# Performance work log

Hardware: AMD Instinct MI355X
Metric: run time of the kernel (lower is better)

## Reference

```python
import jax, jax.numpy as jnp
import numpy as np

EPS = 1e-16  # PyG softmax eps
NEG_SLOPE = 0.2


def _gat_conv(x, W, att_src, att_dst, bias, src, dst, num_nodes, heads, ch, concat):
    # add self loops (PyG default add_self_loops=True)
    loop = jnp.arange(num_nodes, dtype=src.dtype)
    src = jnp.concatenate([src, loop])
    dst = jnp.concatenate([dst, loop])

    h = (x @ W).reshape(num_nodes, heads, ch)          # [N,H,C]
    a_src = jnp.sum(h * att_src, axis=-1)              # [N,H]
    a_dst = jnp.sum(h * att_dst, axis=-1)              # [N,H]

    e = a_src[src] + a_dst[dst]                        # [E,H]
    e = jnp.where(e > 0, e, NEG_SLOPE * e)             # leaky_relu

    # segment softmax over edges grouped by destination node
    m = jax.ops.segment_max(e, dst, num_segments=num_nodes)
    e = jnp.exp(e - m[dst])
    s = jax.ops.segment_sum(e, dst, num_segments=num_nodes)
    alpha = e / (s[dst] + EPS)                          # [E,H]

    msg = h[src] * alpha[:, :, None]                    # [E,H,C]
    out = jax.ops.segment_sum(msg, dst, num_segments=num_nodes)  # [N,H,C]

    if concat:
        out = out.reshape(num_nodes, heads * ch)
    else:
        out = out.mean(axis=1)
    return out + bias


def setup_inputs() -> dict:
    key = jax.random.key(0)
    ks = jax.random.split(key, 12)
    N, E = 50000, 800000
    C_in, C_hid, C_out, H = 128, 32, 64, 8

    x = jax.random.normal(ks[0], (N, C_in), dtype=jnp.float32)
    edge_index = jax.random.randint(ks[1], (2, E), 0, N, dtype=jnp.int64)
    edge_weight = jax.random.uniform(ks[2], (E,), dtype=jnp.float32)

    g = lambda k, shape, fan: jax.random.normal(k, shape, dtype=jnp.float32) * (1.0 / np.sqrt(fan))
    W1 = g(ks[3], (C_in, H * C_hid), C_in)
    att_src1 = g(ks[4], (H, C_hid), C_hid)
    att_dst1 = g(ks[5], (H, C_hid), C_hid)
    bias1 = jnp.zeros((H * C_hid,), dtype=jnp.float32)
    W2 = g(ks[6], (H * C_hid, C_out), H * C_hid)
    att_src2 = g(ks[7], (1, C_out), C_out)
    att_dst2 = g(ks[8], (1, C_out), C_out)
    bias2 = jnp.zeros((C_out,), dtype=jnp.float32)

    return {"x": x, "edge_index": edge_index, "edge_weight": edge_weight,
            "W1": W1, "att_src1": att_src1, "att_dst1": att_dst1, "bias1": bias1,
            "W2": W2, "att_src2": att_src2, "att_dst2": att_dst2, "bias2": bias2}


def reference(x, edge_index, edge_weight, W1, att_src1, att_dst1, bias1,
              W2, att_src2, att_dst2, bias2):
    N = x.shape[0]
    src, dst = edge_index[0], edge_index[1]
    # edge_weight is ignored: GATConv has edge_dim=None, so edge_attr contributes nothing
    h = _gat_conv(x, W1, att_src1, att_dst1, bias1, src, dst, N, 8, 32, concat=True)
    h = jax.nn.elu(h)
    out = _gat_conv(h, W2, att_src2, att_dst2, bias2, src, dst, N, 1, 64, concat=False)
    return out
```

## Files before the change

kernel.cpp:

```cpp
#include <hip/hip_runtime.h>
#include <hip/hip_fp16.h>
#include <math.h>


#define LEAKY(e) ((e) > 0.f ? (e) : 0.2f * (e))
#define CAP 64
#define NPART 2
#define NPB 25000
#define NPW 12500
#define CS 16384

struct __align__(8) H4 { __half2 a, b; };

typedef _Float16 half8 __attribute__((ext_vector_type(8)));
typedef float f32x4 __attribute__((ext_vector_type(4)));

__global__ __launch_bounds__(256) void k1_kernel(
    const int* __restrict__ ei, unsigned* __restrict__ Hg,
    const float* __restrict__ x,
    const float* __restrict__ W1, _Float16* __restrict__ h1h,
    const float* __restrict__ att_src1, const float* __restrict__ att_dst1,
    float* __restrict__ a_src1, float* __restrict__ a_dst1, int N, int E,
    int B, int hblocks) {
  __shared__ __align__(16) unsigned sraw[NPW];
  int t = threadIdx.x, b = blockIdx.x;
  if (b < hblocks) {
    int chunk = b >> 1, p = b & 1;
    for (int i = t; i < NPW; i += 256) sraw[i] = 0u;
    __syncthreads();
    int base = chunk * CS;
    int pbase = p * NPB;
    for (int j = 0; j < CS; j += 256) {
      int idx = base + j + t;
      if (idx < E) {
        int d = ei[E + idx];
        unsigned dl = (unsigned)(d - pbase);
        if (dl < NPB) atomicAdd(&sraw[dl >> 1], 1u << ((dl & 1) * 16));
      }
    }
    __syncthreads();
    unsigned* Hs = Hg + (size_t)(p * B + chunk) * NPW;
    for (int i = t; i < NPW; i += 256) Hs[i] = sraw[i];
    return;
  }
  _Float16* Bs = (_Float16*)sraw;
  int bx = b - hblocks;
  int cb = bx & 3;
  int c0 = cb * 64;
  int w = t >> 6, l = t & 63;
  int lm = l & 15, lq = l >> 4;
  {
    int n = t & 63;
    int kw = t >> 6;
#pragma unroll 8
    for (int i = 0; i < 32; i++) {
      int k = i * 4 + kw;
      Bs[n * 136 + k] = (_Float16)W1[k * 256 + c0 + n];
    }
  }
  __syncthreads();
  int m0 = (bx >> 2) * 128 + w * 32;
  int ra = m0 + lm;      if (ra > N - 1) ra = N - 1;
  int rb = m0 + 16 + lm; if (rb > N - 1) rb = N - 1;
  f32x4 acc[2][4];
#pragma unroll
  for (int mt = 0; mt < 2; mt++)
#pragma unroll
    for (int nt = 0; nt < 4; nt++) acc[mt][nt] = (f32x4){0.f, 0.f, 0.f, 0.f};
  for (int k0 = 0; k0 < 128; k0 += 32) {
    const float* pa = x + (size_t)ra * 128 + k0 + lq * 8;
    const float* pb = x + (size_t)rb * 128 + k0 + lq * 8;
    float4 u0 = *(const float4*)pa, u1 = *(const float4*)(pa + 4);
    float4 w0 = *(const float4*)pb, w1 = *(const float4*)(pb + 4);
    half8 a0, a1;
    a0[0] = (_Float16)u0.x; a0[1] = (_Float16)u0.y;
    a0[2] = (_Float16)u0.z; a0[3] = (_Float16)u0.w;
    a0[4] = (_Float16)u1.x; a0[5] = (_Float16)u1.y;
    a0[6] = (_Float16)u1.z; a0[7] = (_Float16)u1.w;
    a1[0] = (_Float16)w0.x; a1[1] = (_Float16)w0.y;
    a1[2] = (_Float16)w0.z; a1[3] = (_Float16)w0.w;
    a1[4] = (_Float16)w1.x; a1[5] = (_Float16)w1.y;
    a1[6] = (_Float16)w1.z; a1[7] = (_Float16)w1.w;
    half8 b0 = *(const half8*)(Bs + (0 + lm) * 136 + k0 + lq * 8);
    half8 b1 = *(const half8*)(Bs + (16 + lm) * 136 + k0 + lq * 8);
    half8 b2 = *(const half8*)(Bs + (32 + lm) * 136 + k0 + lq * 8);
    half8 b3 = *(const half8*)(Bs + (48 + lm) * 136 + k0 + lq * 8);
    acc[0][0] = __builtin_amdgcn_mfma_f32_16x16x32_f16(a0, b0, acc[0][0], 0, 0, 0);
    acc[0][1] = __builtin_amdgcn_mfma_f32_16x16x32_f16(a0, b1, acc[0][1], 0, 0, 0);
    acc[0][2] = __builtin_amdgcn_mfma_f32_16x16x32_f16(a0, b2, acc[0][2], 0, 0, 0);
    acc[0][3] = __builtin_amdgcn_mfma_f32_16x16x32_f16(a0, b3, acc[0][3], 0, 0, 0);
    acc[1][0] = __builtin_amdgcn_mfma_f32_16x16x32_f16(a1, b0, acc[1][0], 0, 0, 0);
    acc[1][1] = __builtin_amdgcn_mfma_f32_16x16x32_f16(a1, b1, acc[1][1], 0, 0, 0);
    acc[1][2] = __builtin_amdgcn_mfma_f32_16x16x32_f16(a1, b2, acc[1][2], 0, 0, 0);
    acc[1][3] = __builtin_amdgcn_mfma_f32_16x16x32_f16(a1, b3, acc[1][3], 0, 0, 0);
  }
  float as_[4], ad_[4];
#pragma unroll
  for (int nt = 0; nt < 4; nt++) {
    as_[nt] = att_src1[c0 + nt * 16 + lm];
    ad_[nt] = att_dst1[c0 + nt * 16 + lm];
  }
#pragma unroll
  for (int mt = 0; mt < 2; mt++) {
#pragma unroll
    for (int i = 0; i < 4; i++) {
      int gr = m0 + mt * 16 + lq * 4 + i;
      bool ok = gr < N;
      if (ok) {
#pragma unroll
        for (int nt = 0; nt < 4; nt++)
          h1h[(size_t)gr * 256 + c0 + nt * 16 + lm] = (_Float16)acc[mt][nt][i];
      }
      float p0 = acc[mt][0][i] * as_[0] + acc[mt][1][i] * as_[1];
      float p1 = acc[mt][2][i] * as_[2] + acc[mt][3][i] * as_[3];
      float q0 = acc[mt][0][i] * ad_[0] + acc[mt][1][i] * ad_[1];
      float q1 = acc[mt][2][i] * ad_[2] + acc[mt][3][i] * ad_[3];
#pragma unroll
      for (int o = 1; o < 16; o <<= 1) {
        p0 += __shfl_xor(p0, o, 64);
        p1 += __shfl_xor(p1, o, 64);
        q0 += __shfl_xor(q0, o, 64);
        q1 += __shfl_xor(q1, o, 64);
      }
      if (lm == 0 && ok) {
        int h0 = c0 >> 5;
        a_src1[(size_t)gr * 8 + h0] = p0;
        a_src1[(size_t)gr * 8 + h0 + 1] = p1;
        a_dst1[(size_t)gr * 8 + h0] = q0;
        a_dst1[(size_t)gr * 8 + h0 + 1] = q1;
      }
    }
  }
}

__global__ __launch_bounds__(256) void prefix_kernel(
    unsigned* __restrict__ Hg, int* __restrict__ deg,
    int* __restrict__ csr_src, int N, int B) {
  int wid = blockIdx.x * 256 + threadIdx.x;
  if (wid >= NPART * NPW) return;
  int p = wid / NPW, w0 = wid - p * NPW;
  unsigned* Hp = Hg + (size_t)p * B * NPW + w0;
  unsigned lo = 0, hi = 0;
  for (int b = 0; b < B; b++) {
    unsigned v = Hp[(size_t)b * NPW];
    Hp[(size_t)b * NPW] = lo | (hi << 16);
    lo += v & 0xffffu;
    hi += v >> 16;
  }
  int d0 = p * NPB + 2 * w0, d1 = d0 + 1;
  if (d0 < N) { deg[d0] = (int)lo; csr_src[(size_t)d0 * CAP] = d0; }
  if (d1 < N) { deg[d1] = (int)hi; csr_src[(size_t)d1 * CAP] = d1; }
}

__global__ __launch_bounds__(256) void scatter_kernel(
    const int* __restrict__ ei, const unsigned* __restrict__ Hg,
    int* __restrict__ csr_src, int E, int B) {
  __shared__ unsigned cnt[NPW];
  int t = threadIdx.x, b = blockIdx.x;
  int chunk = b >> 1, p = b & 1;
  const unsigned* Hs = Hg + (size_t)(p * B + chunk) * NPW;
  for (int i = t; i < NPW; i += 256) cnt[i] = Hs[i];
  __syncthreads();
  int base = chunk * CS;
  int pbase = p * NPB;
  for (int j = 0; j < CS; j += 256) {
    int idx = base + j + t;
    if (idx < E) {
      int s = ei[idx];
      int d = ei[E + idx];
      unsigned dl = (unsigned)(d - pbase);
      if (dl < NPB) {
        unsigned sh = (dl & 1) * 16;
        unsigned old = atomicAdd(&cnt[dl >> 1], 1u << sh);
        int slot = 1 + (int)((old >> sh) & 0xffffu);
        if (slot < CAP) csr_src[(size_t)d * CAP + slot] = s;
      }
    }
  }
}

__global__ __launch_bounds__(256) void agg1_kernel(
    const int* __restrict__ deg, const int* __restrict__ csr_src,
    const float* __restrict__ a_src1, const float* __restrict__ a_dst1,
    const __half* __restrict__ h1h, const float* __restrict__ bias,
    _Float16* __restrict__ h_act, int n) {
  int w = threadIdx.x >> 6, l = threadIdx.x & 63;
  int hh = l >> 3;
  int c4 = 4 * l;
  float4 bb = *(const float4*)(bias + c4);
  int nw = gridDim.x * 4;
  for (int d = blockIdx.x * 4 + w; d < n; d += nw) {
    int cnt = deg[d] + 1;
    if (cnt > CAP) cnt = CAP;
    const int* sp = csr_src + (size_t)d * CAP;
    float adst = a_dst1[(size_t)d * 8 + hh];
    float4 acc = make_float4(0.f, 0.f, 0.f, 0.f);
    float p = 0.f;
    int i = 0;
    for (; i + 8 <= cnt; i += 8) {
      int s[8];
      H4 v[8];
      float xv[8];
#pragma unroll
      for (int j = 0; j < 8; j++) s[j] = sp[i + j];
#pragma unroll
      for (int j = 0; j < 8; j++)
        v[j] = *(const H4*)(h1h + (size_t)s[j] * 256 + c4);
#pragma unroll
      for (int j = 0; j < 8; j++) {
        float e = a_src1[(size_t)s[j] * 8 + hh] + adst;
        e = LEAKY(e);
        xv[j] = __expf(e);
        p += xv[j];
      }
#pragma unroll
      for (int j = 0; j < 8; j++) {
        float2 p0 = __half22float2(v[j].a), p1 = __half22float2(v[j].b);
        acc.x = fmaf(p0.x, xv[j], acc.x);
        acc.y = fmaf(p0.y, xv[j], acc.y);
        acc.z = fmaf(p1.x, xv[j], acc.z);
        acc.w = fmaf(p1.y, xv[j], acc.w);
      }
    }
    for (; i < cnt; i++) {
      int s = sp[i];
      float e = a_src1[(size_t)s * 8 + hh] + adst;
      e = LEAKY(e);
      float a = __expf(e);
      p += a;
      H4 v = *(const H4*)(h1h + (size_t)s * 256 + c4);
      float2 p0 = __half22float2(v.a), p1 = __half22float2(v.b);
      acc.x = fmaf(p0.x, a, acc.x);
      acc.y = fmaf(p0.y, a, acc.y);
      acc.z = fmaf(p1.x, a, acc.z);
      acc.w = fmaf(p1.y, a, acc.w);
    }
    float rinv = 1.f / (p + 1e-16f);
    float ox = fmaf(acc.x, rinv, bb.x), oy = fmaf(acc.y, rinv, bb.y);
    float oz = fmaf(acc.z, rinv, bb.z), ow = fmaf(acc.w, rinv, bb.w);
    ox = ox > 0.f ? ox : expm1f(ox);
    oy = oy > 0.f ? oy : expm1f(oy);
    oz = oz > 0.f ? oz : expm1f(oz);
    ow = ow > 0.f ? ow : expm1f(ow);
    H4 hv;
    hv.a = __floats2half2_rn(ox, oy);
    hv.b = __floats2half2_rn(oz, ow);
    *(H4*)(h_act + (size_t)d * 256 + c4) = hv;
  }
}

__global__ __launch_bounds__(256) void gemm2_kernel(
    const _Float16* __restrict__ h_act, const float* __restrict__ W2,
    _Float16* __restrict__ h2h, const float* __restrict__ att_src2,
    const float* __restrict__ att_dst2, float* __restrict__ a_src2,
    float* __restrict__ a_dst2, int N) {
  __shared__ _Float16 Bs[64 * 264];
  int t = threadIdx.x;
  int w = t >> 6, l = t & 63;
  int lm = l & 15, lq = l >> 4;
  {
    int n = t & 63;
    int kw = t >> 6;
#pragma unroll 8
    for (int i = 0; i < 64; i++) {
      int k = i * 4 + kw;
      Bs[n * 264 + k] = (_Float16)W2[k * 64 + n];
    }
  }
  __syncthreads();
  const int K = 256;
  int m0 = blockIdx.x * 128 + w * 32;
  int ra = m0 + lm;      if (ra > N - 1) ra = N - 1;
  int rb = m0 + 16 + lm; if (rb > N - 1) rb = N - 1;
  f32x4 acc[2][4];
#pragma unroll
  for (int mt = 0; mt < 2; mt++)
#pragma unroll
    for (int nt = 0; nt < 4; nt++) acc[mt][nt] = (f32x4){0.f, 0.f, 0.f, 0.f};
  for (int k0 = 0; k0 < K; k0 += 32) {
    half8 a0 = *(const half8*)(h_act + (size_t)ra * K + k0 + lq * 8);
    half8 a1 = *(const half8*)(h_act + (size_t)rb * K + k0 + lq * 8);
    half8 b0 = *(const half8*)(Bs + (0 + lm) * 264 + k0 + lq * 8);
    half8 b1 = *(const half8*)(Bs + (16 + lm) * 264 + k0 + lq * 8);
    half8 b2 = *(const half8*)(Bs + (32 + lm) * 264 + k0 + lq * 8);
    half8 b3 = *(const half8*)(Bs + (48 + lm) * 264 + k0 + lq * 8);
    acc[0][0] = __builtin_amdgcn_mfma_f32_16x16x32_f16(a0, b0, acc[0][0], 0, 0, 0);
    acc[0][1] = __builtin_amdgcn_mfma_f32_16x16x32_f16(a0, b1, acc[0][1], 0, 0, 0);
    acc[0][2] = __builtin_amdgcn_mfma_f32_16x16x32_f16(a0, b2, acc[0][2], 0, 0, 0);
    acc[0][3] = __builtin_amdgcn_mfma_f32_16x16x32_f16(a0, b3, acc[0][3], 0, 0, 0);
    acc[1][0] = __builtin_amdgcn_mfma_f32_16x16x32_f16(a1, b0, acc[1][0], 0, 0, 0);
    acc[1][1] = __builtin_amdgcn_mfma_f32_16x16x32_f16(a1, b1, acc[1][1], 0, 0, 0);
    acc[1][2] = __builtin_amdgcn_mfma_f32_16x16x32_f16(a1, b2, acc[1][2], 0, 0, 0);
    acc[1][3] = __builtin_amdgcn_mfma_f32_16x16x32_f16(a1, b3, acc[1][3], 0, 0, 0);
  }
  float as_[4], ad_[4];
#pragma unroll
  for (int nt = 0; nt < 4; nt++) {
    as_[nt] = att_src2[nt * 16 + lm];
    ad_[nt] = att_dst2[nt * 16 + lm];
  }
#pragma unroll
  for (int mt = 0; mt < 2; mt++) {
#pragma unroll
    for (int i = 0; i < 4; i++) {
      int gr = m0 + mt * 16 + lq * 4 + i;
      bool ok = gr < N;
      if (ok) {
#pragma unroll
        for (int nt = 0; nt < 4; nt++)
          h2h[(size_t)gr * 64 + nt * 16 + lm] = (_Float16)acc[mt][nt][i];
      }
      float p0 = acc[mt][0][i] * as_[0] + acc[mt][1][i] * as_[1];
      float p1 = acc[mt][2][i] * as_[2] + acc[mt][3][i] * as_[3];
      float q0 = acc[mt][0][i] * ad_[0] + acc[mt][1][i] * ad_[1];
      float q1 = acc[mt][2][i] * ad_[2] + acc[mt][3][i] * ad_[3];
#pragma unroll
      for (int o = 1; o < 16; o <<= 1) {
        p0 += __shfl_xor(p0, o, 64);
        p1 += __shfl_xor(p1, o, 64);
        q0 += __shfl_xor(q0, o, 64);
        q1 += __shfl_xor(q1, o, 64);
      }
      if (lm == 0 && ok) {
        a_src2[gr] = p0 + p1;
        a_dst2[gr] = q0 + q1;
      }
    }
  }
}

__global__ __launch_bounds__(256) void agg2_kernel(
    const int* __restrict__ deg, const int* __restrict__ csr_src,
    const float* __restrict__ a_src2, const float* __restrict__ a_dst2,
    const __half* __restrict__ h2h, const float* __restrict__ bias,
    float* __restrict__ out, int n) {
  int w = threadIdx.x >> 6, l = threadIdx.x & 63;
  int e2 = l >> 5;
  int c2 = (l & 31) * 2;
  float2 bb = *(const float2*)(bias + c2);
  int nw = gridDim.x * 4;
  for (int d = blockIdx.x * 4 + w; d < n; d += nw) {
    int cnt = deg[d] + 1;
    if (cnt > CAP) cnt = CAP;
    const int* sp = csr_src + (size_t)d * CAP;
    float adst = a_dst2[d];
    float2 acc = make_float2(0.f, 0.f);
    float p = 0.f;
    int i = 0;
    for (; i + 16 <= cnt; i += 16) {
      int s[8];
      __half2 v[8];
      float xv[8];
#pragma unroll
      for (int j = 0; j < 8; j++) s[j] = sp[i + j * 2 + e2];
#pragma unroll
      for (int j = 0; j < 8; j++)
        v[j] = *(const __half2*)(h2h + (size_t)s[j] * 64 + c2);
#pragma unroll
      for (int j = 0; j < 8; j++) {
        float e = a_src2[s[j]] + adst;
        e = LEAKY(e);
        xv[j] = __expf(e);
        p += xv[j];
      }
#pragma unroll
      for (int j = 0; j < 8; j++) {
        float2 f = __half22float2(v[j]);
        acc.x = fmaf(f.x, xv[j], acc.x);
        acc.y = fmaf(f.y, xv[j], acc.y);
      }
    }
    for (; i + e2 < cnt; i += 2) {
      int s = sp[i + e2];
      float e = a_src2[s] + adst;
      e = LEAKY(e);
      float a = __expf(e);
      p += a;
      float2 f = __half22float2(*(const __half2*)(h2h + (size_t)s * 64 + c2));
      acc.x = fmaf(f.x, a, acc.x);
      acc.y = fmaf(f.y, a, acc.y);
    }
    float sx = acc.x + __shfl_xor(acc.x, 32, 64);
    float sy = acc.y + __shfl_xor(acc.y, 32, 64);
    float pp = p + __shfl_xor(p, 32, 64);
    if (l < 32) {
      float rinv = 1.f / (pp + 1e-16f);
      *(float2*)(out + (size_t)d * 64 + c2) =
          make_float2(fmaf(sx, rinv, bb.x), fmaf(sy, rinv, bb.y));
    }
  }
}

extern "C" void kernel_launch(void* const* d_in, const int* in_sizes, int n_in,
                              void* d_out, int out_size, void* d_ws, size_t ws_size,
                              hipStream_t stream) {
  const float* x        = (const float*)d_in[0];
  const int*   ei       = (const int*)d_in[1];
  const float* W1       = (const float*)d_in[3];
  const float* att_src1 = (const float*)d_in[4];
  const float* att_dst1 = (const float*)d_in[5];
  const float* bias1    = (const float*)d_in[6];
  const float* W2       = (const float*)d_in[7];
  const float* att_src2 = (const float*)d_in[8];
  const float* att_dst2 = (const float*)d_in[9];
  const float* bias2    = (const float*)d_in[10];
  float* out = (float*)d_out;

  int N = in_sizes[0] / 128;
  int E = in_sizes[1] / 2;

  char* ws = (char*)d_ws;
  size_t off = 0;
  auto carve = [&](size_t bytes) -> void* {
    void* p = ws + off;
    off += (bytes + 255) & ~(size_t)255;
    return p;
  };
  _Float16* h1h   = (_Float16*)carve((size_t)N * 256 * 2);
  _Float16* h2h   = (_Float16*)carve((size_t)N * 64 * 2);
  _Float16* h_act = (_Float16*)carve((size_t)N * 256 * 2);
  float* a_src1  = (float*)carve((size_t)N * 8 * 4);
  float* a_dst1  = (float*)carve((size_t)N * 8 * 4);
  float* a_src2  = (float*)carve((size_t)N * 4);
  float* a_dst2  = (float*)carve((size_t)N * 4);
  int* deg       = (int*)carve((size_t)N * 4);
  int* csr_src   = (int*)carve((size_t)N * CAP * 4);
  (void)ws_size; (void)n_in; (void)out_size;

  int B = (E + CS - 1) / CS;
  int hblocks = B * NPART;
  unsigned* Hg = (unsigned*)h_act;

  int gblocks = ((N + 127) / 128) * 4;
  k1_kernel<<<hblocks + gblocks, 256, 0, stream>>>(
      ei, Hg, x, W1, h1h, att_src1, att_dst1, a_src1, a_dst1, N, E, B,
      hblocks);
  int pwords = NPART * NPW;
  prefix_kernel<<<(pwords + 255) / 256, 256, 0, stream>>>(Hg, deg, csr_src, N, B);
  scatter_kernel<<<hblocks, 256, 0, stream>>>(ei, Hg, csr_src, E, B);
  agg1_kernel<<<2048, 256, 0, stream>>>(
      deg, csr_src, a_src1, a_dst1, (const __half*)h1h, bias1, h_act, N);
  gemm2_kernel<<<(N + 127) / 128, 256, 0, stream>>>(
      h_act, W2, h2h, att_src2, att_dst2, a_src2, a_dst2, N);
  agg2_kernel<<<2048, 256, 0, stream>>>(
      deg, csr_src, a_src2, a_dst2, (const __half*)h2h, bias2, out, N);
}
```

Before: 303.0 us.

## Repartition histogram into four parts, widen GEMM1 tiles, one-node-per-wave aggregation

The histogram/scatter pass is split into four destination partitions with smaller edge chunks, which shrinks shared memory and produces more blocks. The first GEMM now computes 128 output columns per block instead of 64, halving the number of GEMM blocks and reusing each loaded x tile across twice as many MFMAs, at the cost of more accumulator registers. The two aggregation kernels drop their grid-stride loops and launch one wave per destination node. The added launch overhead of the larger grids and the higher register pressure may offset the gains.

```diff
diff --git a/kernel.cpp b/kernel.cpp
--- a/kernel.cpp
+++ b/kernel.cpp
@@ -5,10 +5,10 @@
 
 #define LEAKY(e) ((e) > 0.f ? (e) : 0.2f * (e))
 #define CAP 64
-#define NPART 2
-#define NPB 25000
-#define NPW 12500
-#define CS 16384
+#define NPART 4
+#define NPB 12500
+#define NPW 6250
+#define CS 8192
 
 struct __align__(8) H4 { __half2 a, b; };
 
@@ -22,10 +22,10 @@
     const float* __restrict__ att_src1, const float* __restrict__ att_dst1,
     float* __restrict__ a_src1, float* __restrict__ a_dst1, int N, int E,
     int B, int hblocks) {
-  __shared__ __align__(16) unsigned sraw[NPW];
+  __shared__ __align__(16) unsigned sraw[8704];
   int t = threadIdx.x, b = blockIdx.x;
   if (b < hblocks) {
-    int chunk = b >> 1, p = b & 1;
+    int chunk = b >> 2, p = b & 3;
     for (int i = t; i < NPW; i += 256) sraw[i] = 0u;
     __syncthreads();
     int base = chunk * CS;
@@ -45,28 +45,28 @@
   }
   _Float16* Bs = (_Float16*)sraw;
   int bx = b - hblocks;
-  int cb = bx & 3;
-  int c0 = cb * 64;
+  int cb = bx & 1;
+  int c0 = cb * 128;
   int w = t >> 6, l = t & 63;
   int lm = l & 15, lq = l >> 4;
   {
-    int n = t & 63;
-    int kw = t >> 6;
+    int n = t & 127;
+    int kw = t >> 7;
 #pragma unroll 8
-    for (int i = 0; i < 32; i++) {
-      int k = i * 4 + kw;
+    for (int i = 0; i < 64; i++) {
+      int k = i * 2 + kw;
       Bs[n * 136 + k] = (_Float16)W1[k * 256 + c0 + n];
     }
   }
   __syncthreads();
-  int m0 = (bx >> 2) * 128 + w * 32;
+  int m0 = (bx >> 1) * 128 + w * 32;
   int ra = m0 + lm;      if (ra > N - 1) ra = N - 1;
   int rb = m0 + 16 + lm; if (rb > N - 1) rb = N - 1;
-  f32x4 acc[2][4];
+  f32x4 acc[2][8];
 #pragma unroll
   for (int mt = 0; mt < 2; mt++)
 #pragma unroll
-    for (int nt = 0; nt < 4; nt++) acc[mt][nt] = (f32x4){0.f, 0.f, 0.f, 0.f};
+    for (int nt = 0; nt < 8; nt++) acc[mt][nt] = (f32x4){0.f, 0.f, 0.f, 0.f};
   for (int k0 = 0; k0 < 128; k0 += 32) {
     const float* pa = x + (size_t)ra * 128 + k0 + lq * 8;
     const float* pb = x + (size_t)rb * 128 + k0 + lq * 8;
@@ -81,22 +81,16 @@
     a1[2] = (_Float16)w0.z; a1[3] = (_Float16)w0.w;
     a1[4] = (_Float16)w1.x; a1[5] = (_Float16)w1.y;
     a1[6] = (_Float16)w1.z; a1[7] = (_Float16)w1.w;
-    half8 b0 = *(const half8*)(Bs + (0 + lm) * 136 + k0 + lq * 8);
-    half8 b1 = *(const half8*)(Bs + (16 + lm) * 136 + k0 + lq * 8);
-    half8 b2 = *(const half8*)(Bs + (32 + lm) * 136 + k0 + lq * 8);
-    half8 b3 = *(const half8*)(Bs + (48 + lm) * 136 + k0 + lq * 8);
-    acc[0][0] = __builtin_amdgcn_mfma_f32_16x16x32_f16(a0, b0, acc[0][0], 0, 0, 0);
-    acc[0][1] = __builtin_amdgcn_mfma_f32_16x16x32_f16(a0, b1, acc[0][1], 0, 0, 0);
-    acc[0][2] = __builtin_amdgcn_mfma_f32_16x16x32_f16(a0, b2, acc[0][2], 0, 0, 0);
-    acc[0][3] = __builtin_amdgcn_mfma_f32_16x16x32_f16(a0, b3, acc[0][3], 0, 0, 0);
-    acc[1][0] = __builtin_amdgcn_mfma_f32_16x16x32_f16(a1, b0, acc[1][0], 0, 0, 0);
-    acc[1][1] = __builtin_amdgcn_mfma_f32_16x16x32_f16(a1, b1, acc[1][1], 0, 0, 0);
-    acc[1][2] = __builtin_amdgcn_mfma_f32_16x16x32_f16(a1, b2, acc[1][2], 0, 0, 0);
-    acc[1][3] = __builtin_amdgcn_mfma_f32_16x16x32_f16(a1, b3, acc[1][3], 0, 0, 0);
-  }
-  float as_[4], ad_[4];
-#pragma unroll
-  for (int nt = 0; nt < 4; nt++) {
+#pragma unroll
+    for (int nt = 0; nt < 8; nt++) {
+      half8 bv = *(const half8*)(Bs + (nt * 16 + lm) * 136 + k0 + lq * 8);
+      acc[0][nt] = __builtin_amdgcn_mfma_f32_16x16x32_f16(a0, bv, acc[0][nt], 0, 0, 0);
+      acc[1][nt] = __builtin_amdgcn_mfma_f32_16x16x32_f16(a1, bv, acc[1][nt], 0, 0, 0);
+    }
+  }
+  float as_[8], ad_[8];
+#pragma unroll
+  for (int nt = 0; nt < 8; nt++) {
     as_[nt] = att_src1[c0 + nt * 16 + lm];
     ad_[nt] = att_dst1[c0 + nt * 16 + lm];
   }
@@ -108,26 +102,32 @@
       bool ok = gr < N;
       if (ok) {
 #pragma unroll
-        for (int nt = 0; nt < 4; nt++)
+        for (int nt = 0; nt < 8; nt++)
           h1h[(size_t)gr * 256 + c0 + nt * 16 + lm] = (_Float16)acc[mt][nt][i];
       }
-      float p0 = acc[mt][0][i] * as_[0] + acc[mt][1][i] * as_[1];
-      float p1 = acc[mt][2][i] * as_[2] + acc[mt][3][i] * as_[3];
-      float q0 = acc[mt][0][i] * ad_[0] + acc[mt][1][i] * ad_[1];
-      float q1 = acc[mt][2][i] * ad_[2] + acc[mt][3][i] * ad_[3];
+      float ph[4], qh[4];
+#pragma unroll
+      for (int hb = 0; hb < 4; hb++) {
+        ph[hb] = acc[mt][2 * hb][i] * as_[2 * hb] +
+                 acc[mt][2 * hb + 1][i] * as_[2 * hb + 1];
+        qh[hb] = acc[mt][2 * hb][i] * ad_[2 * hb] +
+                 acc[mt][2 * hb + 1][i] * ad_[2 * hb + 1];
+      }
 #pragma unroll
       for (int o = 1; o < 16; o <<= 1) {
-        p0 += __shfl_xor(p0, o, 64);
-        p1 += __shfl_xor(p1, o, 64);
-        q0 += __shfl_xor(q0, o, 64);
-        q1 += __shfl_xor(q1, o, 64);
+#pragma unroll
+        for (int hb = 0; hb < 4; hb++) {
+          ph[hb] += __shfl_xor(ph[hb], o, 64);
+          qh[hb] += __shfl_xor(qh[hb], o, 64);
+        }
       }
       if (lm == 0 && ok) {
-        int h0 = c0 >> 5;
-        a_src1[(size_t)gr * 8 + h0] = p0;
-        a_src1[(size_t)gr * 8 + h0 + 1] = p1;
-        a_dst1[(size_t)gr * 8 + h0] = q0;
-        a_dst1[(size_t)gr * 8 + h0 + 1] = q1;
+        int h0 = cb * 4;
+#pragma unroll
+        for (int hb = 0; hb < 4; hb++) {
+          a_src1[(size_t)gr * 8 + h0 + hb] = ph[hb];
+          a_dst1[(size_t)gr * 8 + h0 + hb] = qh[hb];
+        }
       }
     }
   }
@@ -157,7 +157,7 @@
     int* __restrict__ csr_src, int E, int B) {
   __shared__ unsigned cnt[NPW];
   int t = threadIdx.x, b = blockIdx.x;
-  int chunk = b >> 1, p = b & 1;
+  int chunk = b >> 2, p = b & 3;
   const unsigned* Hs = Hg + (size_t)(p * B + chunk) * NPW;
   for (int i = t; i < NPW; i += 256) cnt[i] = Hs[i];
   __syncthreads();
@@ -185,68 +185,66 @@
     const __half* __restrict__ h1h, const float* __restrict__ bias,
     _Float16* __restrict__ h_act, int n) {
   int w = threadIdx.x >> 6, l = threadIdx.x & 63;
+  int d = blockIdx.x * 4 + w;
+  if (d >= n) return;
+  int cnt = deg[d] + 1;
+  if (cnt > CAP) cnt = CAP;
+  const int* sp = csr_src + (size_t)d * CAP;
   int hh = l >> 3;
-  int c4 = 4 * l;
-  float4 bb = *(const float4*)(bias + c4);
-  int nw = gridDim.x * 4;
-  for (int d = blockIdx.x * 4 + w; d < n; d += nw) {
-    int cnt = deg[d] + 1;
-    if (cnt > CAP) cnt = CAP;
-    const int* sp = csr_src + (size_t)d * CAP;
-    float adst = a_dst1[(size_t)d * 8 + hh];
-    float4 acc = make_float4(0.f, 0.f, 0.f, 0.f);
-    float p = 0.f;
-    int i = 0;
-    for (; i + 8 <= cnt; i += 8) {
-      int s[8];
-      H4 v[8];
-      float xv[8];
-#pragma unroll
-      for (int j = 0; j < 8; j++) s[j] = sp[i + j];
-#pragma unroll
-      for (int j = 0; j < 8; j++)
-        v[j] = *(const H4*)(h1h + (size_t)s[j] * 256 + c4);
-#pragma unroll
-      for (int j = 0; j < 8; j++) {
-        float e = a_src1[(size_t)s[j] * 8 + hh] + adst;
-        e = LEAKY(e);
-        xv[j] = __expf(e);
-        p += xv[j];
-      }
-#pragma unroll
-      for (int j = 0; j < 8; j++) {
-        float2 p0 = __half22float2(v[j].a), p1 = __half22float2(v[j].b);
-        acc.x = fmaf(p0.x, xv[j], acc.x);
-        acc.y = fmaf(p0.y, xv[j], acc.y);
-        acc.z = fmaf(p1.x, xv[j], acc.z);
-        acc.w = fmaf(p1.y, xv[j], acc.w);
-      }
-    }
-    for (; i < cnt; i++) {
-      int s = sp[i];
-      float e = a_src1[(size_t)s * 8 + hh] + adst;
+  float adst = a_dst1[(size_t)d * 8 + hh];
+  float4 acc = make_float4(0.f, 0.f, 0.f, 0.f);
+  float p = 0.f;
+  int i = 0;
+  for (; i + 8 <= cnt; i += 8) {
+    int s[8];
+    H4 v[8];
+    float xv[8];
+#pragma unroll
+    for (int j = 0; j < 8; j++) s[j] = sp[i + j];
+#pragma unroll
+    for (int j = 0; j < 8; j++)
+      v[j] = *(const H4*)(h1h + (size_t)s[j] * 256 + 4 * l);
+#pragma unroll
+    for (int j = 0; j < 8; j++) {
+      float e = a_src1[(size_t)s[j] * 8 + hh] + adst;
       e = LEAKY(e);
-      float a = __expf(e);
-      p += a;
-      H4 v = *(const H4*)(h1h + (size_t)s * 256 + c4);
-      float2 p0 = __half22float2(v.a), p1 = __half22float2(v.b);
-      acc.x = fmaf(p0.x, a, acc.x);
-      acc.y = fmaf(p0.y, a, acc.y);
-      acc.z = fmaf(p1.x, a, acc.z);
-      acc.w = fmaf(p1.y, a, acc.w);
-    }
-    float rinv = 1.f / (p + 1e-16f);
-    float ox = fmaf(acc.x, rinv, bb.x), oy = fmaf(acc.y, rinv, bb.y);
-    float oz = fmaf(acc.z, rinv, bb.z), ow = fmaf(acc.w, rinv, bb.w);
-    ox = ox > 0.f ? ox : expm1f(ox);
-    oy = oy > 0.f ? oy : expm1f(oy);
-    oz = oz > 0.f ? oz : expm1f(oz);
-    ow = ow > 0.f ? ow : expm1f(ow);
-    H4 hv;
-    hv.a = __floats2half2_rn(ox, oy);
-    hv.b = __floats2half2_rn(oz, ow);
-    *(H4*)(h_act + (size_t)d * 256 + c4) = hv;
-  }
+      xv[j] = __expf(e);
+      p += xv[j];
+    }
+#pragma unroll
+    for (int j = 0; j < 8; j++) {
+      float2 p0 = __half22float2(v[j].a), p1 = __half22float2(v[j].b);
+      acc.x = fmaf(p0.x, xv[j], acc.x);
+      acc.y = fmaf(p0.y, xv[j], acc.y);
+      acc.z = fmaf(p1.x, xv[j], acc.z);
+      acc.w = fmaf(p1.y, xv[j], acc.w);
+    }
+  }
+  for (; i < cnt; i++) {
+    int s = sp[i];
+    float e = a_src1[(size_t)s * 8 + hh] + adst;
+    e = LEAKY(e);
+    float a = __expf(e);
+    p += a;
+    H4 v = *(const H4*)(h1h + (size_t)s * 256 + 4 * l);
+    float2 p0 = __half22float2(v.a), p1 = __half22float2(v.b);
+    acc.x = fmaf(p0.x, a, acc.x);
+    acc.y = fmaf(p0.y, a, acc.y);
+    acc.z = fmaf(p1.x, a, acc.z);
+    acc.w = fmaf(p1.y, a, acc.w);
+  }
+  float rinv = 1.f / (p + 1e-16f);
+  float4 b = *(const float4*)(bias + 4 * l);
+  float ox = fmaf(acc.x, rinv, b.x), oy = fmaf(acc.y, rinv, b.y);
+  float oz = fmaf(acc.z, rinv, b.z), ow = fmaf(acc.w, rinv, b.w);
+  ox = ox > 0.f ? ox : expm1f(ox);
+  oy = oy > 0.f ? oy : expm1f(oy);
+  oz = oz > 0.f ? oz : expm1f(oz);
+  ow = ow > 0.f ? ow : expm1f(ow);
+  H4 hv;
+  hv.a = __floats2half2_rn(ox, oy);
+  hv.b = __floats2half2_rn(oz, ow);
+  *(H4*)(h_act + (size_t)d * 256 + 4 * l) = hv;
 }
 
 __global__ __launch_bounds__(256) void gemm2_kernel(
@@ -335,59 +333,58 @@
     const __half* __restrict__ h2h, const float* __restrict__ bias,
     float* __restrict__ out, int n) {
   int w = threadIdx.x >> 6, l = threadIdx.x & 63;
+  int d = blockIdx.x * 4 + w;
+  if (d >= n) return;
+  int cnt = deg[d] + 1;
+  if (cnt > CAP) cnt = CAP;
+  const int* sp = csr_src + (size_t)d * CAP;
+  float adst = a_dst2[d];
   int e2 = l >> 5;
   int c2 = (l & 31) * 2;
-  float2 bb = *(const float2*)(bias + c2);
-  int nw = gridDim.x * 4;
-  for (int d = blockIdx.x * 4 + w; d < n; d += nw) {
-    int cnt = deg[d] + 1;
-    if (cnt > CAP) cnt = CAP;
-    const int* sp = csr_src + (size_t)d * CAP;
-    float adst = a_dst2[d];
-    float2 acc = make_float2(0.f, 0.f);
-    float p = 0.f;
-    int i = 0;
-    for (; i + 16 <= cnt; i += 16) {
-      int s[8];
-      __half2 v[8];
-      float xv[8];
-#pragma unroll
-      for (int j = 0; j < 8; j++) s[j] = sp[i + j * 2 + e2];
-#pragma unroll
-      for (int j = 0; j < 8; j++)
-        v[j] = *(const __half2*)(h2h + (size_t)s[j] * 64 + c2);
-#pragma unroll
-      for (int j = 0; j < 8; j++) {
-        float e = a_src2[s[j]] + adst;
-        e = LEAKY(e);
-        xv[j] = __expf(e);
-        p += xv[j];
-      }
-#pragma unroll
-      for (int j = 0; j < 8; j++) {
-        float2 f = __half22float2(v[j]);
-        acc.x = fmaf(f.x, xv[j], acc.x);
-        acc.y = fmaf(f.y, xv[j], acc.y);
-      }
-    }
-    for (; i + e2 < cnt; i += 2) {
-      int s = sp[i + e2];
-      float e = a_src2[s] + adst;
+  float2 acc = make_float2(0.f, 0.f);
+  float p = 0.f;
+  int i = 0;
+  for (; i + 16 <= cnt; i += 16) {
+    int s[8];
+    __half2 v[8];
+    float xv[8];
+#pragma unroll
+    for (int j = 0; j < 8; j++) s[j] = sp[i + j * 2 + e2];
+#pragma unroll
+    for (int j = 0; j < 8; j++)
+      v[j] = *(const __half2*)(h2h + (size_t)s[j] * 64 + c2);
+#pragma unroll
+    for (int j = 0; j < 8; j++) {
+      float e = a_src2[s[j]] + adst;
       e = LEAKY(e);
-      float a = __expf(e);
-      p += a;
-      float2 f = __half22float2(*(const __half2*)(h2h + (size_t)s * 64 + c2));
-      acc.x = fmaf(f.x, a, acc.x);
-      acc.y = fmaf(f.y, a, acc.y);
-    }
-    float sx = acc.x + __shfl_xor(acc.x, 32, 64);
-    float sy = acc.y + __shfl_xor(acc.y, 32, 64);
-    float pp = p + __shfl_xor(p, 32, 64);
-    if (l < 32) {
-      float rinv = 1.f / (pp + 1e-16f);
-      *(float2*)(out + (size_t)d * 64 + c2) =
-          make_float2(fmaf(sx, rinv, bb.x), fmaf(sy, rinv, bb.y));
-    }
+      xv[j] = __expf(e);
+      p += xv[j];
+    }
+#pragma unroll
+    for (int j = 0; j < 8; j++) {
+      float2 f = __half22float2(v[j]);
+      acc.x = fmaf(f.x, xv[j], acc.x);
+      acc.y = fmaf(f.y, xv[j], acc.y);
+    }
+  }
+  for (; i + e2 < cnt; i += 2) {
+    int s = sp[i + e2];
+    float e = a_src2[s] + adst;
+    e = LEAKY(e);
+    float a = __expf(e);
+    p += a;
+    float2 f = __half22float2(*(const __half2*)(h2h + (size_t)s * 64 + c2));
+    acc.x = fmaf(f.x, a, acc.x);
+    acc.y = fmaf(f.y, a, acc.y);
+  }
+  acc.x += __shfl_xor(acc.x, 32, 64);
+  acc.y += __shfl_xor(acc.y, 32, 64);
+  p += __shfl_xor(p, 32, 64);
+  if (l < 32) {
+    float rinv = 1.f / (p + 1e-16f);
+    float2 b = *(const float2*)(bias + c2);
+    *(float2*)(out + (size_t)d * 64 + c2) =
+        make_float2(fmaf(acc.x, rinv, b.x), fmaf(acc.y, rinv, b.y));
   }
 }
 
@@ -431,17 +428,17 @@
   int hblocks = B * NPART;
   unsigned* Hg = (unsigned*)h_act;
 
-  int gblocks = ((N + 127) / 128) * 4;
+  int gblocks = ((N + 127) / 128) * 2;
   k1_kernel<<<hblocks + gblocks, 256, 0, stream>>>(
       ei, Hg, x, W1, h1h, att_src1, att_dst1, a_src1, a_dst1, N, E, B,
       hblocks);
   int pwords = NPART * NPW;
   prefix_kernel<<<(pwords + 255) / 256, 256, 0, stream>>>(Hg, deg, csr_src, N, B);
   scatter_kernel<<<hblocks, 256, 0, stream>>>(ei, Hg, csr_src, E, B);
-  agg1_kernel<<<2048, 256, 0, stream>>>(
+  agg1_kernel<<<(N + 3) / 4, 256, 0, stream>>>(
       deg, csr_src, a_src1, a_dst1, (const __half*)h1h, bias1, h_act, N);
   gemm2_kernel<<<(N + 127) / 128, 256, 0, stream>>>(
       h_act, W2, h2h, att_src2, att_dst2, a_src2, a_dst2, N);
-  agg2_kernel<<<2048, 256, 0, stream>>>(
+  agg2_kernel<<<(N + 3) / 4, 256, 0, stream>>>(
       deg, csr_src, a_src2, a_dst2, (const __half*)h2h, bias2, out, N);
 }
```

Measured after the change: 294.0 us. 1.03x faster.
